# Kernel optimization log

Measured on AMD Instinct MI355X. Metric: run time of the kernel, lower is better.

Reference implementation:

```python
import jax, jax.numpy as jnp
import numpy as np

TEMPERATURE = 0.1
EPS = 1e-12  # matches torch F.normalize eps


def _l2_normalize(x, axis=-1):
    n = jnp.sqrt(jnp.sum(x * x, axis=axis, keepdims=True))
    return x / jnp.maximum(n, EPS)


def setup_inputs() -> dict:
    key = jax.random.key(0)
    k1, k2, k3 = jax.random.split(key, 3)
    B, K, D, M = 128, 256, 256, 4
    local_vectors = jax.random.normal(k1, (B, K, D), dtype=jnp.float32)
    prototypes = jax.random.normal(k2, (K * M, D, 1, 1), dtype=jnp.float32)
    concepts_gt = jax.random.randint(k3, (B, K), 0, 2, dtype=jnp.int32)
    return {
        "local_vectors": local_vectors,
        "prototypes": prototypes,
        "concepts_gt": concepts_gt,
        "num_prototypes_per_concept": M,
    }


def reference(local_vectors, prototypes, concepts_gt, num_prototypes_per_concept):
    B, K, D = local_vectors.shape
    M = num_prototypes_per_concept
    protos = prototypes.reshape(K * M, D)  # squeeze(-1).squeeze(-1)
    ln = _l2_normalize(local_vectors)      # (B, K, D)
    pn = _l2_normalize(protos)             # (K*M, D)

    # similarities for every (b, k) query against all prototypes in one GEMM
    sims = jnp.einsum('bkd,pd->bkp', ln, pn) / TEMPERATURE  # (B, K, K*M)

    # logsumexp over all prototypes (shared across the M positives of a concept)
    lse = jax.nn.logsumexp(sims, axis=-1)  # (B, K)

    # sum of positive similarities: prototypes k*M..(k+1)*M-1 for concept k
    # diagonal over the two K axes, summed over m
    pos_sum = jnp.einsum('bkkm->bk', sims.reshape(B, K, K, M))  # (B, K)

    mask = (concepts_gt == 1).astype(sims.dtype)  # (B, K)
    Mf = jnp.asarray(M, sims.dtype)
    total = jnp.sum(mask * (Mf * lse - pos_sum))
    count = Mf * jnp.sum(mask)
    return jnp.where(count > 0, total / jnp.maximum(count, 1.0), jnp.zeros((), sims.dtype))
```

## Files before the change

### kernel.cpp

```cpp
#include <hip/hip_runtime.h>
#include <hip/hip_bf16.h>
#include <stdint.h>

#define KC   256
#define DD   256
#define NPROT 1024
#define NQ   32768

#define OFF_NSEL 0
#define OFF_TOT  8
#define OFF_TICK 16
#define OFF_SEL  256
#define OFF_PN   131328
#define OFF_QN   655616
#define QSLAB    1048576
#define OFF_ACC  17432832
#define ACC_STRIDE 32768

#define LN2F    0.69314718055994531f
#define C10L2E  14.426950408889634f

typedef __bf16 bf16x8 __attribute__((ext_vector_type(8)));
typedef float  f32x16 __attribute__((ext_vector_type(16)));

static __device__ __forceinline__ unsigned short f2bf(float x) {
  __hip_bfloat16 h = __float2bfloat16(x);
  return __builtin_bit_cast(unsigned short, h);
}

__global__ __launch_bounds__(512) void prep_k(const int* __restrict__ gt,
                                              const float* __restrict__ lv,
                                              const float* __restrict__ protos,
                                              unsigned char* __restrict__ ws) {
  const int blk = blockIdx.x;
  const int tid = threadIdx.x;

  if (blk < 128) {
    const int wv = tid >> 6, lane = tid & 63;
    const int r = blk * 8 + wv;
    const float4 v = ((const float4*)protos)[r * 64 + lane];
    float ss = v.x*v.x + v.y*v.y + v.z*v.z + v.w*v.w;
#pragma unroll
    for (int m = 1; m < 64; m <<= 1) ss += __shfl_xor(ss, m, 64);
    const float sc = C10L2E / fmaxf(sqrtf(ss), 1e-12f);
    uint2 p;
    p.x = (unsigned)f2bf(v.x * sc) | ((unsigned)f2bf(v.y * sc) << 16);
    p.y = (unsigned)f2bf(v.z * sc) | ((unsigned)f2bf(v.w * sc) << 16);
    *(uint2*)(ws + OFF_PN + (lane >> 2) * 32768 + r * 32 + (lane & 3) * 8) = p;
    return;
  }

  __shared__ int wcnt[8], wpre[8];
  __shared__ int sbase, btot;
  __shared__ int list[512];

  const int wv   = tid >> 6, lane = tid & 63;
  const int idx  = (blk - 128) * 512 + tid;

  const int selme = (gt[idx] == 1);
  const unsigned long long bal = __ballot(selme);
  if (lane == 0) wcnt[wv] = __popcll(bal);
  __syncthreads();
  if (tid == 0) {
    int tot = 0;
#pragma unroll
    for (int u = 0; u < 8; ++u) { wpre[u] = tot; tot += wcnt[u]; }
    btot  = tot;
    sbase = atomicAdd((int*)(ws + OFF_NSEL), tot);
  }
  __syncthreads();

  const int rank = __popcll(bal & ((1ull << lane) - 1ull));
  if (selme) {
    const int loc = wpre[wv] + rank;
    list[loc] = idx;
    ((int*)(ws + OFF_SEL))[sbase + loc] = idx;
  }
  __syncthreads();

  const int grp = tid >> 4, sub = tid & 15;
  const int nr  = btot, sb = sbase;
  for (int r = grp; r < nr; r += 32) {
    const int qi   = list[r];
    const int slot = sb + r;
    float4 vv[4];
#pragma unroll
    for (int u = 0; u < 4; ++u) vv[u] = ((const float4*)lv)[qi * 64 + u * 16 + sub];
    float ss = 0.0f;
#pragma unroll
    for (int u = 0; u < 4; ++u)
      ss += vv[u].x*vv[u].x + vv[u].y*vv[u].y + vv[u].z*vv[u].z + vv[u].w*vv[u].w;
#pragma unroll
    for (int m = 1; m < 16; m <<= 1) ss += __shfl_xor(ss, m, 64);
    const float sc = 1.0f / fmaxf(sqrtf(ss), 1e-12f);
#pragma unroll
    for (int u = 0; u < 4; ++u) {
      uint2 p;
      p.x = (unsigned)f2bf(vv[u].x * sc) | ((unsigned)f2bf(vv[u].y * sc) << 16);
      p.y = (unsigned)f2bf(vv[u].z * sc) | ((unsigned)f2bf(vv[u].w * sc) << 16);
      *(uint2*)(ws + OFF_QN + (u * 4 + (sub >> 2)) * QSLAB + slot * 32 + (sub & 3) * 8) = p;
    }
  }
}

__global__ __launch_bounds__(256) void main_k(unsigned char* __restrict__ ws) {
  __shared__ __align__(16) unsigned char Aq[64 * 512];

  const int tid  = threadIdx.x;
  const int w    = tid >> 6;
  const int lane = tid & 63;
  const int hi   = lane >> 5;
  const int l31  = lane & 31;

  const int tile = (int)(blockIdx.x & 511);
  const int c    = (int)(blockIdx.x >> 9);

  const int n_sel = *(const int*)(ws + OFF_NSEL);
  const int base  = tile * 64;
  if (base >= n_sel) return;
  const int* sel = (const int*)(ws + OFF_SEL);

  int valid[2], kqr[2];
#pragma unroll
  for (int j = 0; j < 2; ++j) {
    const int slot = base + j * 32 + l31;
    valid[j] = slot < n_sel;
    const int q = valid[j] ? sel[slot] : sel[base];
    kqr[j] = q & (KC - 1);
  }

  const unsigned char* pn = ws + OFF_PN + (c * 128 + w * 32 + l31) * 32 + hi * 16;

  bf16x8 pa[4];
#pragma unroll
  for (int p = 0; p < 4; ++p) pa[p] = *(const bf16x8*)(pn + p * 32768);

  const unsigned char* qn = ws + OFF_QN;
  const int last = n_sel - 1;
#pragma unroll
  for (int i = 0; i < 4; ++i) {
    const int unit = i * 256 + tid;
    const int s = unit >> 6, r = unit & 63;
    const int slot = min(base + r, last);
    const unsigned char* src = qn + s * QSLAB + slot * 32;
    const uint4 d0 = *(const uint4*)(src);
    const uint4 d1 = *(const uint4*)(src + 16);
    const int swz = ((r & 7) << 4) ^ (((r >> 3) & 3) << 7);
    *(uint4*)(Aq + r * 512 + ((s * 32) ^ swz))      = d0;
    *(uint4*)(Aq + r * 512 + ((s * 32 + 16) ^ swz)) = d1;
  }
  __syncthreads();

  f32x16 acc0, acc1;
#pragma unroll
  for (int t = 0; t < 16; ++t) { acc0[t] = 0.0f; acc1[t] = 0.0f; }

  const int bswz = ((l31 & 7) << 4) ^ (((l31 >> 3) & 3) << 7);

#pragma unroll
  for (int k = 0; k < 16; ++k) {
    const bf16x8 a = pa[k & 3];
    pa[k & 3] = *(const bf16x8*)(pn + ((k + 4) & 15) * 32768);
    const int bc = (k * 32 + hi * 16) ^ bswz;
    const bf16x8 b0 = *(const bf16x8*)(Aq + l31 * 512 + bc);
    const bf16x8 b1 = *(const bf16x8*)(Aq + (32 + l31) * 512 + bc);
    acc0 = __builtin_amdgcn_mfma_f32_32x32x16_bf16(a, b0, acc0, 0, 0, 0);
    acc1 = __builtin_amdgcn_mfma_f32_32x32x16_bf16(a, b1, acc1, 0, 0, 0);
  }

  float l_acc[2] = {0.f, 0.f}, p_acc[2] = {0.f, 0.f};
  const int r4base = c * 32 + w * 8 + hi;
#pragma unroll
  for (int j = 0; j < 2; ++j) {
    float l4[4] = {0.f, 0.f, 0.f, 0.f};
    float p4[4] = {0.f, 0.f, 0.f, 0.f};
#pragma unroll
    for (int g = 0; g < 4; ++g) {
      const float pm = (r4base + 2 * g == kqr[j]) ? 1.0f : 0.0f;
#pragma unroll
      for (int t = 0; t < 4; ++t) {
        const float y = (j == 0) ? acc0[g * 4 + t] : acc1[g * 4 + t];
        l4[t] += __builtin_amdgcn_exp2f(y);
        p4[t] = fmaf(pm, y, p4[t]);
      }
    }
    l_acc[j] = (l4[0] + l4[1]) + (l4[2] + l4[3]);
    p_acc[j] = (p4[0] + p4[1]) + (p4[2] + p4[3]);
  }

#pragma unroll
  for (int j = 0; j < 2; ++j) {
    l_acc[j] += __shfl_xor(l_acc[j], 32, 64);
    p_acc[j] += __shfl_xor(p_acc[j], 32, 64);
  }
  if (hi == 0) {
    float2* accb = (float2*)(ws + OFF_ACC) + (c * 4 + w) * ACC_STRIDE;
#pragma unroll
    for (int j = 0; j < 2; ++j) {
      if (valid[j]) {
        const int slot = base + j * 32 + l31;
        float2 v2; v2.x = l_acc[j]; v2.y = p_acc[j];
        accb[slot] = v2;
      }
    }
  }
}

__global__ __launch_bounds__(256) void finish_k(unsigned char* __restrict__ ws,
                                                float* __restrict__ out) {
  __shared__ float accs[4];
  const int n_sel = *(const int*)(ws + OFF_NSEL);
  const int i = blockIdx.x * 256 + threadIdx.x;
  float contrib = 0.0f;
  if (i < n_sel) {
    const float2* a = (const float2*)(ws + OFF_ACC);
    float L = 0.0f, P = 0.0f;
#pragma unroll
    for (int u = 0; u < 32; ++u) {
      const float2 v = a[u * ACC_STRIDE + i];
      L += v.x; P += v.y;
    }
    contrib = LN2F * (4.0f * __builtin_amdgcn_logf(L) - P);
  }
#pragma unroll
  for (int m = 1; m < 64; m <<= 1) contrib += __shfl_xor(contrib, m, 64);
  if ((threadIdx.x & 63) == 0) accs[threadIdx.x >> 6] = contrib;
  __syncthreads();
  if (threadIdx.x == 0) {
    atomicAdd((float*)(ws + OFF_TOT), (accs[0] + accs[1]) + (accs[2] + accs[3]));
    __threadfence();
    const int t = atomicAdd((int*)(ws + OFF_TICK), 1);
    if (t == 127) {
      const float total = atomicAdd((float*)(ws + OFF_TOT), 0.0f);
      out[0] = (n_sel > 0) ? total / (4.0f * (float)n_sel) : 0.0f;
    }
  }
}

extern "C" void kernel_launch(void* const* d_in, const int* in_sizes, int n_in,
                              void* d_out, int out_size, void* d_ws, size_t ws_size,
                              hipStream_t stream) {
  const float* lv     = (const float*)d_in[0];
  const float* protos = (const float*)d_in[1];
  const int*   gt     = (const int*)d_in[2];
  (void)in_sizes; (void)n_in; (void)out_size; (void)ws_size;
  unsigned char* ws = (unsigned char*)d_ws;

  hipMemsetAsync(d_ws, 0, 256, stream);
  prep_k<<<192, 512, 0, stream>>>(gt, lv, protos, ws);
  main_k<<<4096, 256, 0, stream>>>(ws);
  finish_k<<<128, 256, 0, stream>>>(ws, (float*)d_out);
}
```

Before: 40.10 us.

## Split query normalization into own kernel and widen main blocks to 512 threads

Result: faster. 35.98 us (-10.3%).

```diff
diff --git a/kernel.cpp b/kernel.cpp
--- a/kernel.cpp
+++ b/kernel.cpp
@@ -29,7 +29,6 @@
 }
 
 __global__ __launch_bounds__(512) void prep_k(const int* __restrict__ gt,
-                                              const float* __restrict__ lv,
                                               const float* __restrict__ protos,
                                               unsigned char* __restrict__ ws) {
   const int blk = blockIdx.x;
@@ -51,8 +50,7 @@
   }
 
   __shared__ int wcnt[8], wpre[8];
-  __shared__ int sbase, btot;
-  __shared__ int list[512];
+  __shared__ int sbase;
 
   const int wv   = tid >> 6, lane = tid & 63;
   const int idx  = (blk - 128) * 512 + tid;
@@ -65,24 +63,28 @@
     int tot = 0;
 #pragma unroll
     for (int u = 0; u < 8; ++u) { wpre[u] = tot; tot += wcnt[u]; }
-    btot  = tot;
     sbase = atomicAdd((int*)(ws + OFF_NSEL), tot);
   }
   __syncthreads();
 
   const int rank = __popcll(bal & ((1ull << lane) - 1ull));
-  if (selme) {
-    const int loc = wpre[wv] + rank;
-    list[loc] = idx;
-    ((int*)(ws + OFF_SEL))[sbase + loc] = idx;
-  }
-  __syncthreads();
-
-  const int grp = tid >> 4, sub = tid & 15;
-  const int nr  = btot, sb = sbase;
-  for (int r = grp; r < nr; r += 32) {
-    const int qi   = list[r];
-    const int slot = sb + r;
+  if (selme)
+    ((int*)(ws + OFF_SEL))[sbase + wpre[wv] + rank] = idx;
+}
+
+__global__ __launch_bounds__(256) void qnorm_k(const float* __restrict__ lv,
+                                               unsigned char* __restrict__ ws) {
+  const int n_sel = *(const int*)(ws + OFF_NSEL);
+  const int base  = (int)blockIdx.x * 64;
+  if (base >= n_sel) return;
+  const int* sel = (const int*)(ws + OFF_SEL);
+
+  const int grp = threadIdx.x >> 4, sub = threadIdx.x & 15;
+#pragma unroll
+  for (int t = 0; t < 4; ++t) {
+    const int slot = base + grp * 4 + t;
+    if (slot >= n_sel) break;
+    const int qi = sel[slot];
     float4 vv[4];
 #pragma unroll
     for (int u = 0; u < 4; ++u) vv[u] = ((const float4*)lv)[qi * 64 + u * 16 + sub];
@@ -103,11 +105,11 @@
   }
 }
 
-__global__ __launch_bounds__(256) void main_k(unsigned char* __restrict__ ws) {
+__global__ __launch_bounds__(512) void main_k(unsigned char* __restrict__ ws) {
   __shared__ __align__(16) unsigned char Aq[64 * 512];
 
   const int tid  = threadIdx.x;
-  const int w    = tid >> 6;
+  const int wv   = tid >> 6;
   const int lane = tid & 63;
   const int hi   = lane >> 5;
   const int l31  = lane & 31;
@@ -120,16 +122,15 @@
   if (base >= n_sel) return;
   const int* sel = (const int*)(ws + OFF_SEL);
 
-  int valid[2], kqr[2];
+  int kqr[2];
 #pragma unroll
   for (int j = 0; j < 2; ++j) {
     const int slot = base + j * 32 + l31;
-    valid[j] = slot < n_sel;
-    const int q = valid[j] ? sel[slot] : sel[base];
+    const int q = (slot < n_sel) ? sel[slot] : sel[base];
     kqr[j] = q & (KC - 1);
   }
 
-  const unsigned char* pn = ws + OFF_PN + (c * 128 + w * 32 + l31) * 32 + hi * 16;
+  const unsigned char* pn = ws + OFF_PN + (c * 256 + wv * 32 + l31) * 32 + hi * 16;
 
   bf16x8 pa[4];
 #pragma unroll
@@ -138,8 +139,8 @@
   const unsigned char* qn = ws + OFF_QN;
   const int last = n_sel - 1;
 #pragma unroll
-  for (int i = 0; i < 4; ++i) {
-    const int unit = i * 256 + tid;
+  for (int i = 0; i < 2; ++i) {
+    const int unit = i * 512 + tid;
     const int s = unit >> 6, r = unit & 63;
     const int slot = min(base + r, last);
     const unsigned char* src = qn + s * QSLAB + slot * 32;
@@ -168,8 +169,8 @@
     acc1 = __builtin_amdgcn_mfma_f32_32x32x16_bf16(a, b1, acc1, 0, 0, 0);
   }
 
-  float l_acc[2] = {0.f, 0.f}, p_acc[2] = {0.f, 0.f};
-  const int r4base = c * 32 + w * 8 + hi;
+  float l_acc[2], p_acc[2];
+  const int r4base = c * 64 + wv * 8 + hi;
 #pragma unroll
   for (int j = 0; j < 2; ++j) {
     float l4[4] = {0.f, 0.f, 0.f, 0.f};
@@ -193,16 +194,27 @@
     l_acc[j] += __shfl_xor(l_acc[j], 32, 64);
     p_acc[j] += __shfl_xor(p_acc[j], 32, 64);
   }
+
+  __syncthreads();
+  float* red = (float*)Aq;
   if (hi == 0) {
-    float2* accb = (float2*)(ws + OFF_ACC) + (c * 4 + w) * ACC_STRIDE;
 #pragma unroll
     for (int j = 0; j < 2; ++j) {
-      if (valid[j]) {
-        const int slot = base + j * 32 + l31;
-        float2 v2; v2.x = l_acc[j]; v2.y = p_acc[j];
-        accb[slot] = v2;
-      }
-    }
+      const int s = j * 32 + l31;
+      red[(wv * 64 + s) * 2]     = l_acc[j];
+      red[(wv * 64 + s) * 2 + 1] = p_acc[j];
+    }
+  }
+  __syncthreads();
+  if (tid < 64) {
+    float L = 0.f, P = 0.f;
+#pragma unroll
+    for (int u = 0; u < 8; ++u) {
+      L += red[(u * 64 + tid) * 2];
+      P += red[(u * 64 + tid) * 2 + 1];
+    }
+    float2 v2; v2.x = L; v2.y = P;
+    ((float2*)(ws + OFF_ACC))[c * ACC_STRIDE + base + tid] = v2;
   }
 }
 
@@ -216,7 +228,7 @@
     const float2* a = (const float2*)(ws + OFF_ACC);
     float L = 0.0f, P = 0.0f;
 #pragma unroll
-    for (int u = 0; u < 32; ++u) {
+    for (int u = 0; u < 4; ++u) {
       const float2 v = a[u * ACC_STRIDE + i];
       L += v.x; P += v.y;
     }
@@ -247,7 +259,8 @@
   unsigned char* ws = (unsigned char*)d_ws;
 
   hipMemsetAsync(d_ws, 0, 256, stream);
-  prep_k<<<192, 512, 0, stream>>>(gt, lv, protos, ws);
-  main_k<<<4096, 256, 0, stream>>>(ws);
+  prep_k<<<192, 512, 0, stream>>>(gt, protos, ws);
+  qnorm_k<<<512, 256, 0, stream>>>(lv, ws);
+  main_k<<<2048, 512, 0, stream>>>(ws);
   finish_k<<<128, 256, 0, stream>>>(ws, (float*)d_out);
 }
```
